# Kernel tuning notes

Hardware: AMD Instinct MI355X
Metric: run time of the kernel (lower is better)

The kernel has to match this reference:

```python
import jax, jax.numpy as jnp
import numpy as np

L, H, P = 16384, 1024, 512
DT_MIN, DT_MAX = 1e-3, 1e-1
STEP_RESCALE = 1.0


def setup_inputs() -> dict:
    key = jax.random.key(0)
    ks = jax.random.split(key, 7)
    input_sequence = jax.random.normal(ks[0], (L, H), jnp.float32)
    # eigenvalues with negative real part (left half plane), HiPPO-like imag parts
    Lambda_re = -(jax.random.uniform(ks[1], (P,), jnp.float32) * 0.9 + 0.1)
    Lambda_im = jnp.pi * jnp.arange(P, dtype=jnp.float32)
    B = jax.random.normal(ks[2], (P, H, 2), jnp.float32) / jnp.sqrt(2.0 * H)   # real/imag of B_tilde (P,H)
    C = jax.random.normal(ks[3], (H, P, 2), jnp.float32) / jnp.sqrt(2.0 * P)   # real/imag of C_tilde (H,P)
    D = jax.random.normal(ks[4], (H,), jnp.float32)
    u01 = jax.random.uniform(ks[5], (P, 1), jnp.float32)
    log_step = jnp.log(DT_MIN) + u01 * (jnp.log(DT_MAX) - jnp.log(DT_MIN))     # (P,1)
    return dict(input_sequence=input_sequence, Lambda_re=Lambda_re, Lambda_im=Lambda_im,
                B=B, C=C, D=D, log_step=log_step)


def _binop(q_i, q_j):
    # diagonal linear recurrence composition: (A, b) pairs
    A_i, b_i = q_i
    A_j, b_j = q_j
    return A_j * A_i, A_j * b_i + b_j


def reference(input_sequence, Lambda_re, Lambda_im, B, C, D, log_step):
    Lambda = Lambda_re + 1j * Lambda_im                        # (P,) complex64
    B_tilde = B[..., 0] + 1j * B[..., 1]                       # (P,H)
    C_tilde = C[..., 0] + 1j * C[..., 1]                       # (H,P)
    step = STEP_RESCALE * jnp.exp(log_step[:, 0])              # (P,)
    # ZOH discretization
    Lambda_bar = jnp.exp(Lambda * step)                        # (P,)
    B_bar = ((Lambda_bar - 1.0) / Lambda)[:, None] * B_tilde   # (P,H)
    # Bu_elements: (L,P) complex
    Bu = input_sequence.astype(B_bar.dtype) @ B_bar.T
    Lambda_elems = jnp.broadcast_to(Lambda_bar, Bu.shape)      # (L,P)
    # parallel associative scan over the diagonal recurrence x_t = Lambda_bar*x_{t-1} + Bu_t
    _, xs = jax.lax.associative_scan(_binop, (Lambda_elems, Bu))
    ys = 2.0 * (xs @ C_tilde.T).real                           # conj_sym => factor 2, (L,H)
    return ys + D * input_sequence
```

## Files before the change

### kernel.cpp

```cpp
#include <hip/hip_runtime.h>
#include <math.h>

#define L_SEQ 16384
#define H_DIM 1024
#define P_DIM 512
#define N2P   1024
#define KDIM  1024
#define NKT   16
#define CHUNK 64
#define NCHUNK 256

typedef __attribute__((ext_vector_type(8))) short short8;
typedef __attribute__((ext_vector_type(4))) float f32x4;

__device__ __forceinline__ unsigned short f2bf(float f){
    unsigned int u = __float_as_uint(f);
    u = (u + 0x7FFFu + ((u >> 16) & 1u)) >> 16;
    return (unsigned short)u;
}
__device__ __forceinline__ float bf2f(unsigned int lo16){
    return __uint_as_float(lo16 << 16);
}

__global__ void k_prep_lambda(const float* __restrict__ lre, const float* __restrict__ lim,
                              const float* __restrict__ lstep,
                              float* __restrict__ lam, float* __restrict__ coef,
                              float* __restrict__ lpow)
{
    int p = threadIdx.x;
    double step = exp((double)lstep[p]);
    double dr = (double)lre[p], di = (double)lim[p];
    double ar = dr*step, ai = di*step;
    double er = exp(ar);
    double lbr = er*cos(ai), lbi = er*sin(ai);
    lam[2*p] = (float)lbr; lam[2*p+1] = (float)lbi;
    double nr = lbr - 1.0, ni = lbi;
    double d2 = dr*dr + di*di;
    coef[2*p]   = (float)((nr*dr + ni*di)/d2);
    coef[2*p+1] = (float)((ni*dr - nr*di)/d2);
    double xr = lbr, xi = lbi;
    #pragma unroll
    for (int s=0;s<6;s++){ double t = xr*xr - xi*xi; xi = 2.0*xr*xi; xr = t; }
    lpow[2*p] = (float)xr; lpow[2*p+1] = (float)xi;
}

__global__ __launch_bounds__(256)
void k_prep_bc(const float* __restrict__ B, const float* __restrict__ C,
               const float* __restrict__ coef,
               unsigned short* __restrict__ BB, unsigned short* __restrict__ CC)
{
    int bid = blockIdx.x;
    if (bid < 2048){
        int i = bid*256 + threadIdx.x;
        int p = i >> 10, h = i & 1023;
        float br = B[2*i], bi = B[2*i+1];
        float cr = coef[2*p], ci = coef[2*p+1];
        BB[(size_t)(2*p)*H_DIM + h]   = f2bf(cr*br - ci*bi);
        BB[(size_t)(2*p+1)*H_DIM + h] = f2bf(cr*bi + ci*br);
    } else {
        int i = (bid-2048)*256 + threadIdx.x;
        int h = i >> 9, p = i & 511;
        float cr = C[2*i], ci = C[2*i+1];
        CC[(size_t)h*N2P + 2*p]     = f2bf(2.f*cr);
        CC[(size_t)h*N2P + 2*p + 1] = f2bf(-2.f*ci);
    }
}

__global__ __launch_bounds__(256)
void k_cast(const float4* __restrict__ u, unsigned short* __restrict__ o)
{
    int i = blockIdx.x*256 + threadIdx.x;
    float4 a = u[2*i], b = u[2*i+1];
    union { short8 v; unsigned short s[8]; } r;
    r.s[0]=f2bf(a.x); r.s[1]=f2bf(a.y); r.s[2]=f2bf(a.z); r.s[3]=f2bf(a.w);
    r.s[4]=f2bf(b.x); r.s[5]=f2bf(b.y); r.s[6]=f2bf(b.z); r.s[7]=f2bf(b.w);
    *reinterpret_cast<short8*>(o + (size_t)i*8) = r.v;
}

template<int EPI>
__global__ __launch_bounds__(256, 2)
void gemm128(const unsigned short* __restrict__ A, const unsigned short* __restrict__ Bm,
             float* __restrict__ Cf, unsigned short* __restrict__ Cb,
             const float* __restrict__ Dv, const unsigned short* __restrict__ U16)
{
    __shared__ char lds[65536];
    const int tid  = threadIdx.x;
    const int lane = tid & 63;
    const int wid  = tid >> 6;
    const int wm = wid >> 1, wn = wid & 1;
    const int wg = ((int)blockIdx.x & 7) * 128 + ((int)blockIdx.x >> 3);
    const int tm = wg >> 3, tn = wg & 7;
    const int lr = lane & 15;

    const int srow = tid >> 3;
    const int scol = ((tid & 7) ^ ((tid >> 3) & 7)) << 3;
    const int kc0 = (((lane >> 4)      ^ (lr & 7)) << 4);
    const int kc1 = ((((lane >> 4) | 4) ^ (lr & 7)) << 4);
    const int aOff = (wm*64 + lr)*128;
    const int bOff = 16384 + (wn*64 + lr)*128;

#define GLOAD(SRC, DST) __builtin_amdgcn_global_load_lds( \
        (const __attribute__((address_space(1))) void*)(SRC), \
        (__attribute__((address_space(3))) void*)(DST), 16, 0, 0)
#define STAGE(kt_) do{ \
    char* d_ = lds + (((kt_)&1)<<15) + tid*16; \
    const unsigned short* sa = A + (size_t)(tm*128 + srow)*KDIM + (size_t)(kt_)*64 + scol; \
    GLOAD(sa,                    d_); \
    GLOAD(sa + (size_t)32*KDIM,  d_ + 4096); \
    GLOAD(sa + (size_t)64*KDIM,  d_ + 8192); \
    GLOAD(sa + (size_t)96*KDIM,  d_ + 12288); \
    const unsigned short* sb = Bm + (size_t)(tn*128 + srow)*KDIM + (size_t)(kt_)*64 + scol; \
    GLOAD(sb,                    d_ + 16384); \
    GLOAD(sb + (size_t)32*KDIM,  d_ + 20480); \
    GLOAD(sb + (size_t)64*KDIM,  d_ + 24576); \
    GLOAD(sb + (size_t)96*KDIM,  d_ + 28672); }while(0)
#define RD(OFF) (*(const short8*)(lds + (OFF)))
#define MFMA(a,b,c) __builtin_amdgcn_mfma_f32_16x16x32_bf16(a,b,c,0,0,0)
#define LGKM(N) do{ asm volatile("s_waitcnt lgkmcnt(" #N ")" ::: "memory"); \
                    __builtin_amdgcn_sched_barrier(0); }while(0)
#define ABAR  asm volatile("s_barrier" ::: "memory")

    f32x4 acc[4][4];
    #pragma unroll
    for (int m=0;m<4;m++)
        #pragma unroll
        for (int n=0;n<4;n++) acc[m][n] = (f32x4){0.f,0.f,0.f,0.f};

    STAGE(0); STAGE(1);

    for (int kt = 0; kt < NKT; ++kt) {
        const int sb = (kt & 1) << 15;
        const int tN = (kt+2 < NKT) ? kt+2 : NKT-2+((kt+2)&1);
        asm volatile("s_waitcnt vmcnt(8)" ::: "memory");
        ABAR;
        short8 a0[4], b0[4], a1v[4], b1v[4];
        #pragma unroll
        for (int m=0;m<4;m++) a0[m] = RD(sb + aOff + m*2048 + kc0);
        #pragma unroll
        for (int n=0;n<4;n++) b0[n] = RD(sb + bOff + n*2048 + kc0);
        STAGE(tN);
        #pragma unroll
        for (int m=0;m<4;m++) a1v[m] = RD(sb + aOff + m*2048 + kc1);
        #pragma unroll
        for (int n=0;n<4;n++) b1v[n] = RD(sb + bOff + n*2048 + kc1);
        LGKM(8);
        #pragma unroll
        for (int m=0;m<4;m++)
            #pragma unroll
            for (int n=0;n<4;n++) acc[m][n] = MFMA(a0[m], b0[n], acc[m][n]);
        LGKM(0);
        #pragma unroll
        for (int m=0;m<4;m++)
            #pragma unroll
            for (int n=0;n<4;n++) acc[m][n] = MFMA(a1v[m], b1v[n], acc[m][n]);
    }
    asm volatile("s_waitcnt vmcnt(0)" ::: "memory");

    const int orow0 = tm*128 + wm*64 + (lane>>4)*4;
    const int ocol0 = tn*128 + wn*64 + lr;
    #pragma unroll
    for (int m=0;m<4;m++){
        #pragma unroll
        for (int n=0;n<4;n++){
            int row = orow0 + m*16, col = ocol0 + n*16;
            #pragma unroll
            for (int j=0;j<4;j++){
                size_t idx = (size_t)(row + j)*N2P + col;
                if (EPI) Cf[idx] = acc[m][n][j] + Dv[col]*bf2f(U16[idx]);
                else     Cb[idx] = f2bf(acc[m][n][j]);
            }
        }
    }
#undef GLOAD
#undef STAGE
#undef RD
#undef MFMA
#undef LGKM
#undef ABAR
}

__global__ __launch_bounds__(512)
void k_agg(const unsigned int* __restrict__ Bu, const float* __restrict__ lam,
           float* __restrict__ agg)
{
    int p = threadIdx.x, c = blockIdx.x;
    float lrr = lam[2*p], lii = lam[2*p+1];
    float xr = 0.f, xi = 0.f;
    const unsigned int* b2 = Bu + (size_t)c*CHUNK*512 + p;
    #pragma unroll 4
    for (int t=0;t<CHUNK;t++){
        unsigned int b = b2[(size_t)t*512];
        float br = __uint_as_float(b << 16);
        float bi = __uint_as_float(b & 0xffff0000u);
        float tr = lrr*xr - lii*xi + br;
        xi = lrr*xi + lii*xr + bi;
        xr = tr;
    }
    agg[((size_t)c*P_DIM + p)*2]     = xr;
    agg[((size_t)c*P_DIM + p)*2 + 1] = xi;
}

__global__ __launch_bounds__(256)
void k_scan(const float* __restrict__ agg, const float* __restrict__ lpow,
            float* __restrict__ xinit)
{
    __shared__ float sr[NCHUNK], si[NCHUNK];
    int c = threadIdx.x, p = blockIdx.x;
    float xr = agg[((size_t)c*P_DIM + p)*2];
    float xi = agg[((size_t)c*P_DIM + p)*2 + 1];
    sr[c] = xr; si[c] = xi;
    float wr = lpow[2*p], wi = lpow[2*p+1];
    for (int s=1; s<NCHUNK; s<<=1){
        __syncthreads();
        float ur = 0.f, ui = 0.f;
        if (c >= s){ ur = sr[c-s]; ui = si[c-s]; }
        __syncthreads();
        xr += wr*ur - wi*ui;
        xi += wr*ui + wi*ur;
        sr[c] = xr; si[c] = xi;
        float t = wr*wr - wi*wi; wi = 2.f*wr*wi; wr = t;
    }
    __syncthreads();
    float er = 0.f, ei = 0.f;
    if (c > 0){ er = sr[c-1]; ei = si[c-1]; }
    xinit[((size_t)c*P_DIM + p)*2]     = er;
    xinit[((size_t)c*P_DIM + p)*2 + 1] = ei;
}

__global__ __launch_bounds__(512)
void k_apply(const unsigned int* __restrict__ Bu, const float* __restrict__ lam,
             const float* __restrict__ xinit, unsigned int* __restrict__ xs)
{
    int p = threadIdx.x, c = blockIdx.x;
    float lrr = lam[2*p], lii = lam[2*p+1];
    float xr = xinit[((size_t)c*P_DIM + p)*2];
    float xi = xinit[((size_t)c*P_DIM + p)*2 + 1];
    const unsigned int* b2 = Bu + (size_t)c*CHUNK*512 + p;
    unsigned int* o = xs + (size_t)c*CHUNK*512 + p;
    #pragma unroll 4
    for (int t=0;t<CHUNK;t++){
        unsigned int b = b2[(size_t)t*512];
        float br = __uint_as_float(b << 16);
        float bi = __uint_as_float(b & 0xffff0000u);
        float tr = lrr*xr - lii*xi + br;
        xi = lrr*xi + lii*xr + bi;
        xr = tr;
        o[(size_t)t*512] = (unsigned int)f2bf(xr) | ((unsigned int)f2bf(xi) << 16);
    }
}

extern "C" void kernel_launch(void* const* d_in, const int* in_sizes, int n_in,
                              void* d_out, int out_size, void* d_ws, size_t ws_size,
                              hipStream_t stream)
{
    const float* u   = (const float*)d_in[0];
    const float* lre = (const float*)d_in[1];
    const float* lim = (const float*)d_in[2];
    const float* B   = (const float*)d_in[3];
    const float* C   = (const float*)d_in[4];
    const float* D   = (const float*)d_in[5];
    const float* ls  = (const float*)d_in[6];
    float* out = (float*)d_out;

    char* w = (char*)d_ws;
    unsigned short* u16  = (unsigned short*)(w + 0);
    unsigned short* xs16 = (unsigned short*)(w + 33554432);
    unsigned short* Bu16 = (unsigned short*)(w + 67108864);
    unsigned short* BB   = (unsigned short*)(w + 100663296);
    unsigned short* CC   = (unsigned short*)(w + 102760448);
    float* lam   = (float*)(w + 104857600);
    float* coef  = (float*)(w + 104861696);
    float* lpow  = (float*)(w + 104865792);
    float* agg   = (float*)(w + 104869888);
    float* xinit = (float*)(w + 105918464);

    k_prep_lambda<<<1, P_DIM, 0, stream>>>(lre, lim, ls, lam, coef, lpow);
    k_prep_bc<<<4096, 256, 0, stream>>>(B, C, coef, BB, CC);
    k_cast<<<(L_SEQ*H_DIM)/(256*8), 256, 0, stream>>>((const float4*)u, u16);

    gemm128<0><<<1024, 256, 0, stream>>>(u16, BB, nullptr, Bu16, nullptr, nullptr);

    k_agg<<<NCHUNK, P_DIM, 0, stream>>>((const unsigned int*)Bu16, lam, agg);
    k_scan<<<P_DIM, NCHUNK, 0, stream>>>(agg, lpow, xinit);
    k_apply<<<NCHUNK, P_DIM, 0, stream>>>((const unsigned int*)Bu16, lam, xinit,
                                          (unsigned int*)xs16);

    gemm128<1><<<1024, 256, 0, stream>>>(xs16, CC, out, nullptr, D, u16);
}
```

Before: 132.7 us.

## Fuse fp32-to-bf16 input cast into first GEMM and simplify its pipeline

This removes the standalone cast kernel and the bf16 copy of the input. The first GEMM now loads fp32 input tiles into registers, converts them to bf16 and writes them into LDS. The second GEMM's epilogue reads the fp32 input directly for the D skip term. The GEMM main loop also changes from a two-deep prefetch with hand-placed waitcnt and barrier to a simpler double-buffer with __syncthreads, and it issues a redundant wrap-around load on the last iteration. The aim is to cut a full read/write pass and a launch, at the cost of reading twice as many A-operand bytes through the GEMM and possibly less load/compute overlap.

```diff
diff --git a/kernel.cpp b/kernel.cpp
--- a/kernel.cpp
+++ b/kernel.cpp
@@ -66,22 +66,12 @@
     }
 }
 
-__global__ __launch_bounds__(256)
-void k_cast(const float4* __restrict__ u, unsigned short* __restrict__ o)
-{
-    int i = blockIdx.x*256 + threadIdx.x;
-    float4 a = u[2*i], b = u[2*i+1];
-    union { short8 v; unsigned short s[8]; } r;
-    r.s[0]=f2bf(a.x); r.s[1]=f2bf(a.y); r.s[2]=f2bf(a.z); r.s[3]=f2bf(a.w);
-    r.s[4]=f2bf(b.x); r.s[5]=f2bf(b.y); r.s[6]=f2bf(b.z); r.s[7]=f2bf(b.w);
-    *reinterpret_cast<short8*>(o + (size_t)i*8) = r.v;
-}
-
-template<int EPI>
+template<int CAST>
 __global__ __launch_bounds__(256, 2)
-void gemm128(const unsigned short* __restrict__ A, const unsigned short* __restrict__ Bm,
+void gemm128(const unsigned short* __restrict__ A16, const float* __restrict__ A32,
+             const unsigned short* __restrict__ Bm,
              float* __restrict__ Cf, unsigned short* __restrict__ Cb,
-             const float* __restrict__ Dv, const unsigned short* __restrict__ U16)
+             const float* __restrict__ Dv, const float* __restrict__ U32)
 {
     __shared__ char lds[65536];
     const int tid  = threadIdx.x;
@@ -93,7 +83,8 @@
     const int lr = lane & 15;
 
     const int srow = tid >> 3;
-    const int scol = ((tid & 7) ^ ((tid >> 3) & 7)) << 3;
+    const int sch  = (tid & 7) ^ ((tid >> 3) & 7);
+    const int scol = sch << 3;
     const int kc0 = (((lane >> 4)      ^ (lr & 7)) << 4);
     const int kc1 = ((((lane >> 4) | 4) ^ (lr & 7)) << 4);
     const int aOff = (wm*64 + lr)*128;
@@ -102,23 +93,25 @@
 #define GLOAD(SRC, DST) __builtin_amdgcn_global_load_lds( \
         (const __attribute__((address_space(1))) void*)(SRC), \
         (__attribute__((address_space(3))) void*)(DST), 16, 0, 0)
-#define STAGE(kt_) do{ \
-    char* d_ = lds + (((kt_)&1)<<15) + tid*16; \
-    const unsigned short* sa = A + (size_t)(tm*128 + srow)*KDIM + (size_t)(kt_)*64 + scol; \
-    GLOAD(sa,                    d_); \
-    GLOAD(sa + (size_t)32*KDIM,  d_ + 4096); \
-    GLOAD(sa + (size_t)64*KDIM,  d_ + 8192); \
-    GLOAD(sa + (size_t)96*KDIM,  d_ + 12288); \
-    const unsigned short* sb = Bm + (size_t)(tn*128 + srow)*KDIM + (size_t)(kt_)*64 + scol; \
-    GLOAD(sb,                    d_ + 16384); \
-    GLOAD(sb + (size_t)32*KDIM,  d_ + 20480); \
-    GLOAD(sb + (size_t)64*KDIM,  d_ + 24576); \
-    GLOAD(sb + (size_t)96*KDIM,  d_ + 28672); }while(0)
 #define RD(OFF) (*(const short8*)(lds + (OFF)))
 #define MFMA(a,b,c) __builtin_amdgcn_mfma_f32_16x16x32_bf16(a,b,c,0,0,0)
-#define LGKM(N) do{ asm volatile("s_waitcnt lgkmcnt(" #N ")" ::: "memory"); \
-                    __builtin_amdgcn_sched_barrier(0); }while(0)
-#define ABAR  asm volatile("s_barrier" ::: "memory")
+
+    auto stage_b = [&](int kt_){
+        char* d_ = lds + ((kt_&1)<<15) + 16384 + tid*16;
+        const unsigned short* sb = Bm + (size_t)(tn*128 + srow)*KDIM + (size_t)kt_*64 + scol;
+        GLOAD(sb,                    d_);
+        GLOAD(sb + (size_t)32*KDIM,  d_ + 4096);
+        GLOAD(sb + (size_t)64*KDIM,  d_ + 8192);
+        GLOAD(sb + (size_t)96*KDIM,  d_ + 12288);
+    };
+    auto stage_a16 = [&](int kt_){
+        char* d_ = lds + ((kt_&1)<<15) + tid*16;
+        const unsigned short* sa = A16 + (size_t)(tm*128 + srow)*KDIM + (size_t)kt_*64 + scol;
+        GLOAD(sa,                    d_);
+        GLOAD(sa + (size_t)32*KDIM,  d_ + 4096);
+        GLOAD(sa + (size_t)64*KDIM,  d_ + 8192);
+        GLOAD(sa + (size_t)96*KDIM,  d_ + 12288);
+    };
 
     f32x4 acc[4][4];
     #pragma unroll
@@ -126,35 +119,58 @@
         #pragma unroll
         for (int n=0;n<4;n++) acc[m][n] = (f32x4){0.f,0.f,0.f,0.f};
 
-    STAGE(0); STAGE(1);
+    float4 av[4][2];
+    auto load_a32 = [&](int kt_){
+        #pragma unroll
+        for (int g=0; g<4; ++g){
+            const float* sa = A32 + (size_t)(tm*128 + g*32 + srow)*KDIM + (size_t)kt_*64 + scol;
+            av[g][0] = *reinterpret_cast<const float4*>(sa);
+            av[g][1] = *reinterpret_cast<const float4*>(sa + 4);
+        }
+    };
+    auto write_a32 = [&](int kt_){
+        #pragma unroll
+        for (int g=0; g<4; ++g){
+            union { short8 v; unsigned short s[8]; } r;
+            r.s[0]=f2bf(av[g][0].x); r.s[1]=f2bf(av[g][0].y);
+            r.s[2]=f2bf(av[g][0].z); r.s[3]=f2bf(av[g][0].w);
+            r.s[4]=f2bf(av[g][1].x); r.s[5]=f2bf(av[g][1].y);
+            r.s[6]=f2bf(av[g][1].z); r.s[7]=f2bf(av[g][1].w);
+            *reinterpret_cast<short8*>(lds + ((kt_&1)<<15) + g*4096 + tid*16) = r.v;
+        }
+    };
+
+    if (CAST){ load_a32(0); write_a32(0); } else { stage_a16(0); }
+    stage_b(0);
+    __syncthreads();
 
     for (int kt = 0; kt < NKT; ++kt) {
         const int sb = (kt & 1) << 15;
-        const int tN = (kt+2 < NKT) ? kt+2 : NKT-2+((kt+2)&1);
-        asm volatile("s_waitcnt vmcnt(8)" ::: "memory");
-        ABAR;
+        const int tN = (kt + 1) & (NKT - 1);
+        if (CAST) load_a32(tN); else stage_a16(tN);
+        stage_b(tN);
+
         short8 a0[4], b0[4], a1v[4], b1v[4];
         #pragma unroll
-        for (int m=0;m<4;m++) a0[m] = RD(sb + aOff + m*2048 + kc0);
-        #pragma unroll
-        for (int n=0;n<4;n++) b0[n] = RD(sb + bOff + n*2048 + kc0);
-        STAGE(tN);
+        for (int m=0;m<4;m++) a0[m]  = RD(sb + aOff + m*2048 + kc0);
+        #pragma unroll
+        for (int n=0;n<4;n++) b0[n]  = RD(sb + bOff + n*2048 + kc0);
         #pragma unroll
         for (int m=0;m<4;m++) a1v[m] = RD(sb + aOff + m*2048 + kc1);
         #pragma unroll
         for (int n=0;n<4;n++) b1v[n] = RD(sb + bOff + n*2048 + kc1);
-        LGKM(8);
         #pragma unroll
         for (int m=0;m<4;m++)
             #pragma unroll
             for (int n=0;n<4;n++) acc[m][n] = MFMA(a0[m], b0[n], acc[m][n]);
-        LGKM(0);
         #pragma unroll
         for (int m=0;m<4;m++)
             #pragma unroll
             for (int n=0;n<4;n++) acc[m][n] = MFMA(a1v[m], b1v[n], acc[m][n]);
-    }
-    asm volatile("s_waitcnt vmcnt(0)" ::: "memory");
+
+        if (CAST) write_a32(tN);
+        __syncthreads();
+    }
 
     const int orow0 = tm*128 + wm*64 + (lane>>4)*4;
     const int ocol0 = tn*128 + wn*64 + lr;
@@ -166,17 +182,14 @@
             #pragma unroll
             for (int j=0;j<4;j++){
                 size_t idx = (size_t)(row + j)*N2P + col;
-                if (EPI) Cf[idx] = acc[m][n][j] + Dv[col]*bf2f(U16[idx]);
-                else     Cb[idx] = f2bf(acc[m][n][j]);
+                if (CAST) Cb[idx] = f2bf(acc[m][n][j]);
+                else      Cf[idx] = acc[m][n][j] + Dv[col]*U32[idx];
             }
         }
     }
 #undef GLOAD
-#undef STAGE
 #undef RD
 #undef MFMA
-#undef LGKM
-#undef ABAR
 }
 
 __global__ __launch_bounds__(512)
@@ -263,27 +276,25 @@
     float* out = (float*)d_out;
 
     char* w = (char*)d_ws;
-    unsigned short* u16  = (unsigned short*)(w + 0);
-    unsigned short* xs16 = (unsigned short*)(w + 33554432);
-    unsigned short* Bu16 = (unsigned short*)(w + 67108864);
-    unsigned short* BB   = (unsigned short*)(w + 100663296);
-    unsigned short* CC   = (unsigned short*)(w + 102760448);
-    float* lam   = (float*)(w + 104857600);
-    float* coef  = (float*)(w + 104861696);
-    float* lpow  = (float*)(w + 104865792);
-    float* agg   = (float*)(w + 104869888);
-    float* xinit = (float*)(w + 105918464);
+    unsigned short* xs16 = (unsigned short*)(w + 0);
+    unsigned short* Bu16 = (unsigned short*)(w + 33554432);
+    unsigned short* BB   = (unsigned short*)(w + 67108864);
+    unsigned short* CC   = (unsigned short*)(w + 69206016);
+    float* lam   = (float*)(w + 71303168);
+    float* coef  = (float*)(w + 71307264);
+    float* lpow  = (float*)(w + 71311360);
+    float* agg   = (float*)(w + 71315456);
+    float* xinit = (float*)(w + 72364032);
 
     k_prep_lambda<<<1, P_DIM, 0, stream>>>(lre, lim, ls, lam, coef, lpow);
     k_prep_bc<<<4096, 256, 0, stream>>>(B, C, coef, BB, CC);
-    k_cast<<<(L_SEQ*H_DIM)/(256*8), 256, 0, stream>>>((const float4*)u, u16);
-
-    gemm128<0><<<1024, 256, 0, stream>>>(u16, BB, nullptr, Bu16, nullptr, nullptr);
+
+    gemm128<1><<<1024, 256, 0, stream>>>(nullptr, u, BB, nullptr, Bu16, nullptr, nullptr);
 
     k_agg<<<NCHUNK, P_DIM, 0, stream>>>((const unsigned int*)Bu16, lam, agg);
     k_scan<<<P_DIM, NCHUNK, 0, stream>>>(agg, lpow, xinit);
     k_apply<<<NCHUNK, P_DIM, 0, stream>>>((const unsigned int*)Bu16, lam, xinit,
                                           (unsigned int*)xs16);
 
-    gemm128<1><<<1024, 256, 0, stream>>>(xs16, CC, out, nullptr, D, u16);
-}
+    gemm128<0><<<1024, 256, 0, stream>>>(xs16, nullptr, CC, out, nullptr, D, u);
+}
```

New measurement: 152.3 us. 14.8% more time.
